# Performance work log

Hardware: AMD Instinct MI355X
Metric: run time of the kernel (lower is better)

The kernel has to match this reference:

```python
import jax, jax.numpy as jnp
import numpy as np

DIM_IN, DIM_OUT, DIM_HID = 1024, 1024, 1024
BATCH = 16384


def setup_inputs() -> dict:
    key = jax.random.key(0)
    k1, k2, k3, k4 = jax.random.split(key, 4)
    x = jax.random.normal(k1, (BATCH, DIM_IN), dtype=jnp.float32)
    # W_slow: Linear(dim_in -> dim_out + 2*dim_hidden + 1)
    W_slow_w = jax.random.normal(k2, (DIM_OUT + 2 * DIM_HID + 1, DIM_IN), dtype=jnp.float32) * (1.0 / np.sqrt(DIM_IN))
    W_slow_b = jax.random.normal(k3, (DIM_OUT + 2 * DIM_HID + 1,), dtype=jnp.float32) * 0.01
    # W_fast: Linear(dim_hidden -> dim_out), weight initialized to zero per module
    W_fast_w = jnp.zeros((DIM_OUT, DIM_HID), dtype=jnp.float32)
    W_fast_b = jax.random.normal(k4, (DIM_OUT,), dtype=jnp.float32) * 0.01
    return {"x": x, "W_slow_w": W_slow_w, "W_slow_b": W_slow_b,
            "W_fast_w": W_fast_w, "W_fast_b": W_fast_b}


def reference(x, W_slow_w, W_slow_b, W_fast_w, W_fast_b):
    B = x.shape[0]
    s = x @ W_slow_w.T + W_slow_b                      # [B, O + 2H + 1]
    k = s[:, :DIM_HID]                                 # [B, H]
    v = s[:, DIM_HID:DIM_HID + DIM_OUT]                # [B, O]
    q = s[:, DIM_HID + DIM_OUT:DIM_HID + DIM_OUT + DIM_HID]  # [B, H]
    lr = jax.nn.sigmoid(s[:, -1:])                     # [B, 1]
    # fast-weight read with softmax key
    v_bar = jax.nn.softmax(k, axis=1) @ W_fast_w.T + W_fast_b  # [B, O]
    # delta-rule outer-product update (batched, normalized by B)
    delta = jnp.einsum('bo,bh->oh', lr * (v - v_bar), jax.nn.sigmoid(k)) / B  # [O, H]
    W_new = W_fast_w + delta
    # read with updated fast weights
    return jax.nn.softmax(q, axis=1) @ W_new.T + W_fast_b  # [B, O]
```

## Files before the change

kernel.cpp:

```cpp
#include <hip/hip_runtime.h>
#include <math.h>

static constexpr int BATCH = 16384;

typedef __attribute__((ext_vector_type(8))) __bf16 bf16x8;
typedef __attribute__((ext_vector_type(4))) float f32x4;

__device__ __forceinline__ float sigm(float x) { return 1.0f / (1.0f + expf(-x)); }

__device__ __forceinline__ unsigned short f2bf(float f) {
  unsigned u = __float_as_uint(f);
  return (unsigned short)((u + 0x7fffu + ((u >> 16) & 1u)) >> 16);
}
__device__ __forceinline__ float bf2f(unsigned short u) {
  return __uint_as_float((unsigned)u << 16);
}

template <int EPI>
__global__ __launch_bounds__(512, 2) void mgemm8(
    const unsigned short* __restrict__ Ag, const unsigned short* __restrict__ Bg,
    int lda, int ldb, const float* __restrict__ bias,
    unsigned short* __restrict__ t0, unsigned short* __restrict__ t1,
    unsigned short* __restrict__ t2, float* __restrict__ Cf,
    const unsigned short* __restrict__ vTin, const float* __restrict__ lrp,
    unsigned short* __restrict__ outT, int ldT) {
  constexpr int NT = 32;
  __shared__ unsigned short As[4 * 8192];
  __shared__ unsigned short Bs[4 * 8192];
  const int tid = threadIdx.x, lane = tid & 63, w = tid >> 6;
  const int lm = lane & 15, kg = lane >> 4;
  const int wm = w >> 2, wn = w & 3;
  const int bm = blockIdx.y * 256, bn = blockIdx.x * 256;
  const int kz = (EPI == 3) ? (blockIdx.z << 10) : 0;
  f32x4 acc[8][4] = {};

  int offA[8], offB[4];
#pragma unroll
  for (int i = 0; i < 8; i++) {
    int r = wm * 128 + i * 16 + lm;
    offA[i] = r * 32 + (((kg + r + (r >> 2)) & 3) << 3);
  }
#pragma unroll
  for (int j = 0; j < 4; j++) {
    int r = wn * 64 + j * 16 + lm;
    offB[j] = r * 32 + (((kg + r + (r >> 2)) & 3) << 3);
  }
  const unsigned short* gA[2];
  const unsigned short* gB[2];
  int ldsoff[2];
#pragma unroll
  for (int i = 0; i < 2; i++) {
    int r = i * 128 + w * 16 + (lane >> 2);
    int q = ((lane & 3) - r - (r >> 2)) & 3;
    gA[i] = Ag + (size_t)(bm + r) * lda + kz + q * 8;
    gB[i] = Bg + (size_t)(bn + r) * ldb + kz + q * 8;
    ldsoff[i] = i * 4096 + w * 512;
  }
  auto stageA = [&](int tt, int buf) {
#pragma unroll
    for (int i = 0; i < 2; i++)
      __builtin_amdgcn_global_load_lds(
          (__attribute__((address_space(1))) void*)(unsigned short*)(gA[i] + tt * 32),
          (__attribute__((address_space(3))) void*)(As + buf * 8192 + ldsoff[i]),
          16, 0, 0);
  };
  auto stageB = [&](int tt, int buf) {
#pragma unroll
    for (int i = 0; i < 2; i++)
      __builtin_amdgcn_global_load_lds(
          (__attribute__((address_space(1))) void*)(unsigned short*)(gB[i] + tt * 32),
          (__attribute__((address_space(3))) void*)(Bs + buf * 8192 + ldsoff[i]),
          16, 0, 0);
  };

  stageA(0, 0); stageB(0, 0);
  stageA(1, 1); stageB(1, 1);
  asm volatile("s_waitcnt vmcnt(4)" ::: "memory");
  __builtin_amdgcn_s_barrier();
  __builtin_amdgcn_sched_barrier(0);

  for (int t = 0; t < NT; ++t) {
    const unsigned short* Ab = As + (t & 3) * 8192;
    const unsigned short* Bb = Bs + (t & 3) * 8192;
    bf16x8 aF[4], bF[4];
#pragma unroll
    for (int i = 0; i < 4; i++) aF[i] = *(const bf16x8*)(Ab + offA[i]);
#pragma unroll
    for (int j = 0; j < 4; j++) bF[j] = *(const bf16x8*)(Bb + offB[j]);
    if (t + 2 < NT) stageA(t + 2, (t + 2) & 3);
    __builtin_amdgcn_s_barrier();
    asm volatile("s_waitcnt lgkmcnt(0)" ::: "memory");
    __builtin_amdgcn_sched_barrier(0);
    __builtin_amdgcn_s_setprio(1);
#pragma unroll
    for (int i = 0; i < 4; i++)
#pragma unroll
      for (int j = 0; j < 4; j++)
        acc[i][j] = __builtin_amdgcn_mfma_f32_16x16x32_bf16(aF[i], bF[j], acc[i][j], 0, 0, 0);
    __builtin_amdgcn_s_setprio(0);
    __builtin_amdgcn_sched_barrier(0);
    __builtin_amdgcn_s_barrier();
    bf16x8 aG[4];
#pragma unroll
    for (int i = 0; i < 4; i++) aG[i] = *(const bf16x8*)(Ab + offA[4 + i]);
    if (t + 2 < NT) stageB(t + 2, (t + 2) & 3);
    __builtin_amdgcn_s_barrier();
    asm volatile("s_waitcnt lgkmcnt(0)" ::: "memory");
    __builtin_amdgcn_sched_barrier(0);
    __builtin_amdgcn_s_setprio(1);
#pragma unroll
    for (int i = 0; i < 4; i++)
#pragma unroll
      for (int j = 0; j < 4; j++)
        acc[4 + i][j] = __builtin_amdgcn_mfma_f32_16x16x32_bf16(aG[i], bF[j], acc[4 + i][j], 0, 0, 0);
    __builtin_amdgcn_s_setprio(0);
    __builtin_amdgcn_sched_barrier(0);
    if (t < NT - 2) { asm volatile("s_waitcnt vmcnt(4)" ::: "memory"); }
    else            { asm volatile("s_waitcnt vmcnt(0)" ::: "memory"); }
    __builtin_amdgcn_s_barrier();
    __builtin_amdgcn_sched_barrier(0);
  }

#pragma unroll
  for (int i = 0; i < 8; i++) {
#pragma unroll
    for (int j = 0; j < 4; j++) {
      const int gcol = bn + wn * 64 + j * 16 + lm;
      const int grow0 = bm + wm * 128 + i * 16 + kg * 4;
      if (EPI == 0) {
        const int which = gcol >> 10;
        unsigned short* dst = which == 0 ? t0 : (which == 1 ? t1 : t2);
        const float bv = bias[gcol];
        ushort4 pk;
        pk.x = f2bf(acc[i][j][0] + bv);
        pk.y = f2bf(acc[i][j][1] + bv);
        pk.z = f2bf(acc[i][j][2] + bv);
        pk.w = f2bf(acc[i][j][3] + bv);
        *(ushort4*)(dst + (size_t)(gcol & 1023) * ldT + grow0) = pk;
      } else if (EPI == 1) {
        const float bv = bias[gcol];
        const float4 l4 = *(const float4*)(lrp + grow0);
        const ushort4 v4 = *(const ushort4*)(vTin + (size_t)gcol * ldT + grow0);
        ushort4 o;
        o.x = f2bf(l4.x * (bf2f(v4.x) - (acc[i][j][0] + bv)));
        o.y = f2bf(l4.y * (bf2f(v4.y) - (acc[i][j][1] + bv)));
        o.z = f2bf(l4.z * (bf2f(v4.z) - (acc[i][j][2] + bv)));
        o.w = f2bf(l4.w * (bf2f(v4.w) - (acc[i][j][3] + bv)));
        *(ushort4*)(outT + (size_t)gcol * ldT + grow0) = o;
      } else if (EPI == 2) {
        const float bv = bias[gcol];
#pragma unroll
        for (int r = 0; r < 4; r++)
          Cf[(size_t)(grow0 + r) * 1024 + gcol] = acc[i][j][r] + bv;
      } else {
        float* dst = Cf + (size_t)blockIdx.z * (1024ull * 1024ull);
#pragma unroll
        for (int r = 0; r < 4; r++)
          dst[(size_t)(grow0 + r) * 1024 + gcol] = acc[i][j][r];
      }
    }
  }
}

template <int EPI>
__global__ __launch_bounds__(256) void mgemm(
    const unsigned short* __restrict__ Ag, const unsigned short* __restrict__ Bg,
    int lda, int ldb, int ksl, const float* __restrict__ bias,
    unsigned short* __restrict__ t0, unsigned short* __restrict__ t1,
    unsigned short* __restrict__ t2, float* __restrict__ Cf,
    const unsigned short* __restrict__ vTin, const float* __restrict__ lrp,
    unsigned short* __restrict__ outT, int ldT) {
  __shared__ unsigned short As[128 * 32];
  __shared__ unsigned short Bs[128 * 32];
  const int tid = threadIdx.x, lane = tid & 63, w = tid >> 6;
  const int lm = lane & 15, kg = lane >> 4;
  const int mh = (w >> 1) * 64, nh = (w & 1) * 64;
  const int bm = blockIdx.y * 128, bn = blockIdx.x * 128;
  const int kstart = blockIdx.z * ksl, kend = kstart + ksl;
  f32x4 acc[4][4] = {};

  int offA[4], offB[4];
#pragma unroll
  for (int i = 0; i < 4; i++) {
    int rA = mh + i * 16 + lm;
    offA[i] = rA * 32 + (((kg + rA + (rA >> 2)) & 3) << 3);
    int rB = nh + i * 16 + lm;
    offB[i] = rB * 32 + (((kg + rB + (rB >> 2)) & 3) << 3);
  }
  int rowS[2], kcS[2];
#pragma unroll
  for (int t = 0; t < 2; t++) {
    int c = (w * 2 + t) * 64 + lane;
    rowS[t] = c >> 2;
    kcS[t] = ((((c & 3) - rowS[t] - (rowS[t] >> 2)) & 3) << 3);
  }

  for (int k0 = kstart; k0 < kend; k0 += 32) {
#pragma unroll
    for (int t = 0; t < 2; t++) {
      __builtin_amdgcn_global_load_lds(
          (__attribute__((address_space(1))) void*)(unsigned short*)(
              Ag + (size_t)(bm + rowS[t]) * lda + k0 + kcS[t]),
          (__attribute__((address_space(3))) void*)(As + (w * 2 + t) * 512), 16, 0, 0);
      __builtin_amdgcn_global_load_lds(
          (__attribute__((address_space(1))) void*)(unsigned short*)(
              Bg + (size_t)(bn + rowS[t]) * ldb + k0 + kcS[t]),
          (__attribute__((address_space(3))) void*)(Bs + (w * 2 + t) * 512), 16, 0, 0);
    }
    __syncthreads();
    bf16x8 aF[4], bF[4];
#pragma unroll
    for (int i = 0; i < 4; i++) {
      aF[i] = *(const bf16x8*)(As + offA[i]);
      bF[i] = *(const bf16x8*)(Bs + offB[i]);
    }
#pragma unroll
    for (int i = 0; i < 4; i++)
#pragma unroll
      for (int j = 0; j < 4; j++)
        acc[i][j] = __builtin_amdgcn_mfma_f32_16x16x32_bf16(aF[i], bF[j], acc[i][j], 0, 0, 0);
    __syncthreads();
  }

#pragma unroll
  for (int i = 0; i < 4; i++) {
#pragma unroll
    for (int j = 0; j < 4; j++) {
      const int gcol = bn + nh + j * 16 + lm;
      const int grow0 = bm + mh + i * 16 + kg * 4;
      if (EPI == 3) {
        float* dst = Cf + (size_t)blockIdx.z * (1024ull * 1024ull);
#pragma unroll
        for (int r = 0; r < 4; r++)
          dst[(size_t)(grow0 + r) * 1024 + gcol] = acc[i][j][r];
      }
    }
  }
}

template <bool DOSIG>
__global__ __launch_bounds__(256) void tsoftmax(
    const unsigned short* __restrict__ in, int ldin,
    unsigned short* __restrict__ rowout,
    unsigned short* __restrict__ sigT, int ldT) {
  __shared__ unsigned short tile[1024 * 16];
  __shared__ float red[16 * 17];
  const int t = threadIdx.x, bl = t & 15, fg = t >> 4;
  const int B0 = blockIdx.x * 16;
  const int f0 = fg * 64;
  float ls = 0.f;
  for (int f = f0; f < f0 + 64; f++) {
    unsigned short u = in[(size_t)f * ldin + B0 + bl];
    tile[f * 16 + bl] = u;
    ls += expf(bf2f(u));
  }
  red[bl * 17 + fg] = ls;
  __syncthreads();
  float tot = 0.f;
#pragma unroll
  for (int g = 0; g < 16; g++) tot += red[bl * 17 + g];
  const float inv = 1.0f / tot;
  for (int fb = f0; fb < f0 + 64; fb += 4) {
    float v[4];
#pragma unroll
    for (int e = 0; e < 4; e++) v[e] = bf2f(tile[(fb + e) * 16 + bl]);
    ushort4 o;
    o.x = f2bf(expf(v[0]) * inv);
    o.y = f2bf(expf(v[1]) * inv);
    o.z = f2bf(expf(v[2]) * inv);
    o.w = f2bf(expf(v[3]) * inv);
    *(ushort4*)(rowout + (size_t)(B0 + bl) * 1024 + fb) = o;
    if (DOSIG) {
#pragma unroll
      for (int e = 0; e < 4; e++)
        sigT[(size_t)(fb + e) * ldT + B0 + bl] = f2bf(sigm(v[e]));
    }
  }
}

__global__ __launch_bounds__(256) void lrx(const float* __restrict__ x,
                                           const float* __restrict__ Wsw,
                                           const float* __restrict__ Wsb,
                                           float* __restrict__ lrOut,
                                           unsigned short* __restrict__ xbf) {
  const int lane = threadIdx.x & 63, w = threadIdx.x >> 6;
  const int b = blockIdx.x * 4 + w;
  const float* xr = x + (size_t)b * 1024;
  const float* wr = Wsw + 3072ull * 1024ull;
  float sum = 0.f;
#pragma unroll
  for (int j = 0; j < 4; j++) {
    int f = lane + 64 * j;
    float4 xv = ((const float4*)xr)[f];
    float4 wv = ((const float4*)wr)[f];
    sum += xv.x * wv.x + xv.y * wv.y + xv.z * wv.z + xv.w * wv.w;
    ushort4 o = {f2bf(xv.x), f2bf(xv.y), f2bf(xv.z), f2bf(xv.w)};
    ((ushort4*)(xbf + (size_t)b * 1024))[f] = o;
  }
#pragma unroll
  for (int o = 32; o; o >>= 1) sum += __shfl_down(sum, o, 64);
  if (lane == 0) lrOut[b] = sigm(sum + Wsb[3072]);
}

__global__ __launch_bounds__(256) void cvt_bf(const float* __restrict__ in,
                                              unsigned short* __restrict__ outp) {
  size_t i = (size_t)blockIdx.x * 256 + threadIdx.x;
  float4 v = ((const float4*)in)[i];
  ushort4 o = {f2bf(v.x), f2bf(v.y), f2bf(v.z), f2bf(v.w)};
  ((ushort4*)outp)[i] = o;
}

template <int NZ>
__global__ __launch_bounds__(256) void wnewk(const float* __restrict__ P,
                                             const float* __restrict__ Wfw,
                                             unsigned short* __restrict__ wnbf) {
  const size_t i = (size_t)blockIdx.x * 256 + threadIdx.x;
  float s = 0.f;
#pragma unroll
  for (int z = 0; z < NZ; z++) s += P[(size_t)z * (1024ull * 1024ull) + i];
  wnbf[i] = f2bf(Wfw[i] + s * (1.0f / 16384.0f));
}

extern "C" void kernel_launch(void* const* d_in, const int* in_sizes, int n_in,
                              void* d_out, int out_size, void* d_ws, size_t ws_size,
                              hipStream_t stream) {
  (void)in_sizes; (void)n_in; (void)out_size;
  const float* x   = (const float*)d_in[0];
  const float* Wsw = (const float*)d_in[1];
  const float* Wsb = (const float*)d_in[2];
  const float* Wfw = (const float*)d_in[3];
  const float* Wfb = (const float*)d_in[4];
  float* out = (float*)d_out;

  const size_t MB = 1ull << 20;
  int nc;
  if      (ws_size >= 216 * MB) nc = 1;
  else if (ws_size >= 164 * MB) nc = 2;
  else if (ws_size >= 122 * MB) nc = 4;
  else                          nc = 8;
  const size_t Bc = BATCH / nc;
  const int BcI = (int)Bc;
  const int zc = 8 / nc;
  const size_t CB = Bc * 1024 * 2;

  char* p = (char*)d_ws;
  size_t off = 0;
  auto alloc = [&](size_t bytes) {
    char* cur = p + off;
    off = (off + bytes + 255) & ~(size_t)255;
    return cur;
  };
  unsigned short* wbf  = (unsigned short*)alloc(3072ull * 1024 * 2);
  unsigned short* wfbf = (unsigned short*)alloc(1024ull * 1024 * 2);
  unsigned short* wnbf = (unsigned short*)alloc(1024ull * 1024 * 2);
  float*          lr   = (float*)alloc(BATCH * 4);
  unsigned short* qsm  = (unsigned short*)alloc((size_t)BATCH * 1024 * 2);

  unsigned short *xbf, *ksm, *kt, *Ut, *vT, *qt, *SKt;
  float* P;
  if (nc == 1) {
    char* rA = alloc(CB);
    char* rB = alloc(CB);
    char* rC = alloc(CB);
    char* rD = alloc(CB);
    char* rE = alloc(CB);
    xbf = (unsigned short*)rA; ksm = (unsigned short*)rA;
    kt  = (unsigned short*)rB; Ut  = (unsigned short*)rB;
    vT  = (unsigned short*)rC;
    qt  = (unsigned short*)rD;
    P   = (float*)rC;
    SKt = (unsigned short*)rE;
  } else {
    P   = (float*)alloc(32 * MB);
    char* rA = alloc(CB);
    char* rB = alloc(CB);
    xbf = (unsigned short*)rA; ksm = (unsigned short*)rA;
    kt  = (unsigned short*)rB; Ut  = (unsigned short*)rB;
    vT  = (unsigned short*)alloc(CB);
    qt  = (unsigned short*)alloc(CB);
    SKt = (unsigned short*)alloc(CB);
  }

  cvt_bf<<<dim3(3072), 256, 0, stream>>>(Wsw, wbf);
  cvt_bf<<<dim3(1024), 256, 0, stream>>>(Wfw, wfbf);

  for (int c = 0; c < nc; c++) {
    const float* xc = x + (size_t)c * Bc * 1024;
    float* lrc = lr + (size_t)c * Bc;
    lrx<<<dim3((unsigned)(Bc / 4)), 256, 0, stream>>>(xc, Wsw, Wsb, lrc, xbf);
    mgemm8<0><<<dim3(12, (unsigned)(Bc / 256)), 512, 0, stream>>>(
        xbf, wbf, 1024, 1024, Wsb, kt, vT, qt, nullptr, nullptr, nullptr,
        nullptr, BcI);
    tsoftmax<true><<<dim3((unsigned)(Bc / 16)), 256, 0, stream>>>(
        kt, BcI, ksm, SKt, BcI);
    tsoftmax<false><<<dim3((unsigned)(Bc / 16)), 256, 0, stream>>>(
        qt, BcI, qsm + (size_t)c * Bc * 1024, nullptr, BcI);
    mgemm8<1><<<dim3(4, (unsigned)(Bc / 256)), 512, 0, stream>>>(
        ksm, wfbf, 1024, 1024, Wfb, nullptr, nullptr, nullptr, nullptr,
        vT, lrc, Ut, BcI);
    if (nc == 1) {
      mgemm8<3><<<dim3(4, 4, 16), 512, 0, stream>>>(
          Ut, SKt, BcI, BcI, nullptr, nullptr, nullptr, nullptr,
          P, nullptr, nullptr, nullptr, BcI);
    } else {
      mgemm<3><<<dim3(8, 8, zc), 256, 0, stream>>>(
          Ut, SKt, BcI, BcI, 2048, nullptr, nullptr, nullptr, nullptr,
          P + (size_t)c * zc * 1024 * 1024, nullptr, nullptr, nullptr, BcI);
    }
  }

  if (nc == 1)
    wnewk<16><<<dim3(1024 * 1024 / 256), 256, 0, stream>>>(P, Wfw, wnbf);
  else
    wnewk<8><<<dim3(1024 * 1024 / 256), 256, 0, stream>>>(P, Wfw, wnbf);

  mgemm8<2><<<dim3(4, BATCH / 256), 512, 0, stream>>>(
      qsm, wnbf, 1024, 1024, Wfb, nullptr, nullptr, nullptr, out,
      nullptr, nullptr, nullptr, 0);
}
```

Measured before the change: 504.4 us.

## Prefetch second A fragment early, merge softmax and convert launches, vectorize wnew

In the main GEMM loop, the second half of the A fragments is now read from LDS together with the first half. The wait uses lgkmcnt(4) so the first MFMA batch can start while those reads are still in flight, and one barrier is dropped. The two softmax launches become one kernel with a 2D grid, the two bf16 conversion launches become one, and the weight-update kernel now processes float4 vectors with a quarter of the blocks. This cuts launch overhead and LDS latency stalls, at the cost of more registers held live and one fewer synchronization point.

Measured after the change: 533.2 us. +5.7%, slower.

```diff
diff --git a/kernel.cpp b/kernel.cpp
--- a/kernel.cpp
+++ b/kernel.cpp
@@ -82,14 +82,16 @@
   for (int t = 0; t < NT; ++t) {
     const unsigned short* Ab = As + (t & 3) * 8192;
     const unsigned short* Bb = Bs + (t & 3) * 8192;
-    bf16x8 aF[4], bF[4];
+    bf16x8 aF[4], bF[4], aG[4];
 #pragma unroll
     for (int i = 0; i < 4; i++) aF[i] = *(const bf16x8*)(Ab + offA[i]);
 #pragma unroll
     for (int j = 0; j < 4; j++) bF[j] = *(const bf16x8*)(Bb + offB[j]);
+#pragma unroll
+    for (int i = 0; i < 4; i++) aG[i] = *(const bf16x8*)(Ab + offA[4 + i]);
     if (t + 2 < NT) stageA(t + 2, (t + 2) & 3);
     __builtin_amdgcn_s_barrier();
-    asm volatile("s_waitcnt lgkmcnt(0)" ::: "memory");
+    asm volatile("s_waitcnt lgkmcnt(4)" ::: "memory");
     __builtin_amdgcn_sched_barrier(0);
     __builtin_amdgcn_s_setprio(1);
 #pragma unroll
@@ -100,11 +102,7 @@
     __builtin_amdgcn_s_setprio(0);
     __builtin_amdgcn_sched_barrier(0);
     __builtin_amdgcn_s_barrier();
-    bf16x8 aG[4];
-#pragma unroll
-    for (int i = 0; i < 4; i++) aG[i] = *(const bf16x8*)(Ab + offA[4 + i]);
     if (t + 2 < NT) stageB(t + 2, (t + 2) & 3);
-    __builtin_amdgcn_s_barrier();
     asm volatile("s_waitcnt lgkmcnt(0)" ::: "memory");
     __builtin_amdgcn_sched_barrier(0);
     __builtin_amdgcn_s_setprio(1);
@@ -238,13 +236,15 @@
   }
 }
 
-template <bool DOSIG>
-__global__ __launch_bounds__(256) void tsoftmax(
-    const unsigned short* __restrict__ in, int ldin,
-    unsigned short* __restrict__ rowout,
+__global__ __launch_bounds__(256) void tsoftmax2(
+    const unsigned short* __restrict__ inK, const unsigned short* __restrict__ inQ,
+    int ldin, unsigned short* __restrict__ outK, unsigned short* __restrict__ outQ,
     unsigned short* __restrict__ sigT, int ldT) {
   __shared__ unsigned short tile[1024 * 16];
   __shared__ float red[16 * 17];
+  const bool isK = blockIdx.y == 0;
+  const unsigned short* in = isK ? inK : inQ;
+  unsigned short* rowout = isK ? outK : outQ;
   const int t = threadIdx.x, bl = t & 15, fg = t >> 4;
   const int B0 = blockIdx.x * 16;
   const int f0 = fg * 64;
@@ -270,7 +270,7 @@
     o.z = f2bf(expf(v[2]) * inv);
     o.w = f2bf(expf(v[3]) * inv);
     *(ushort4*)(rowout + (size_t)(B0 + bl) * 1024 + fb) = o;
-    if (DOSIG) {
+    if (isK) {
 #pragma unroll
       for (int e = 0; e < 4; e++)
         sigT[(size_t)(fb + e) * ldT + B0 + bl] = f2bf(sigm(v[e]));
@@ -302,12 +302,17 @@
   if (lane == 0) lrOut[b] = sigm(sum + Wsb[3072]);
 }
 
-__global__ __launch_bounds__(256) void cvt_bf(const float* __restrict__ in,
-                                              unsigned short* __restrict__ outp) {
-  size_t i = (size_t)blockIdx.x * 256 + threadIdx.x;
-  float4 v = ((const float4*)in)[i];
+__global__ __launch_bounds__(256) void cvt2(const float* __restrict__ a,
+                                            const float* __restrict__ b,
+                                            unsigned short* __restrict__ oa,
+                                            unsigned short* __restrict__ ob) {
+  const bool first = blockIdx.x < 3072;
+  const float* src = first ? a : b;
+  unsigned short* dst = first ? oa : ob;
+  size_t i = (size_t)(first ? blockIdx.x : blockIdx.x - 3072) * 256 + threadIdx.x;
+  float4 v = ((const float4*)src)[i];
   ushort4 o = {f2bf(v.x), f2bf(v.y), f2bf(v.z), f2bf(v.w)};
-  ((ushort4*)outp)[i] = o;
+  ((ushort4*)dst)[i] = o;
 }
 
 template <int NZ>
@@ -315,10 +320,17 @@
                                              const float* __restrict__ Wfw,
                                              unsigned short* __restrict__ wnbf) {
   const size_t i = (size_t)blockIdx.x * 256 + threadIdx.x;
-  float s = 0.f;
-#pragma unroll
-  for (int z = 0; z < NZ; z++) s += P[(size_t)z * (1024ull * 1024ull) + i];
-  wnbf[i] = f2bf(Wfw[i] + s * (1.0f / 16384.0f));
+  float4 s = {0.f, 0.f, 0.f, 0.f};
+#pragma unroll
+  for (int z = 0; z < NZ; z++) {
+    float4 v = ((const float4*)(P + (size_t)z * (1024ull * 1024ull)))[i];
+    s.x += v.x; s.y += v.y; s.z += v.z; s.w += v.w;
+  }
+  float4 wv = ((const float4*)Wfw)[i];
+  const float r = 1.0f / 16384.0f;
+  ushort4 o = {f2bf(wv.x + s.x * r), f2bf(wv.y + s.y * r),
+               f2bf(wv.z + s.z * r), f2bf(wv.w + s.w * r)};
+  ((ushort4*)wnbf)[i] = o;
 }
 
 extern "C" void kernel_launch(void* const* d_in, const int* in_sizes, int n_in,
@@ -381,8 +393,7 @@
     SKt = (unsigned short*)alloc(CB);
   }
 
-  cvt_bf<<<dim3(3072), 256, 0, stream>>>(Wsw, wbf);
-  cvt_bf<<<dim3(1024), 256, 0, stream>>>(Wfw, wfbf);
+  cvt2<<<dim3(4096), 256, 0, stream>>>(Wsw, Wfw, wbf, wfbf);
 
   for (int c = 0; c < nc; c++) {
     const float* xc = x + (size_t)c * Bc * 1024;
@@ -391,10 +402,8 @@
     mgemm8<0><<<dim3(12, (unsigned)(Bc / 256)), 512, 0, stream>>>(
         xbf, wbf, 1024, 1024, Wsb, kt, vT, qt, nullptr, nullptr, nullptr,
         nullptr, BcI);
-    tsoftmax<true><<<dim3((unsigned)(Bc / 16)), 256, 0, stream>>>(
-        kt, BcI, ksm, SKt, BcI);
-    tsoftmax<false><<<dim3((unsigned)(Bc / 16)), 256, 0, stream>>>(
-        qt, BcI, qsm + (size_t)c * Bc * 1024, nullptr, BcI);
+    tsoftmax2<<<dim3((unsigned)(Bc / 16), 2), 256, 0, stream>>>(
+        kt, qt, BcI, ksm, qsm + (size_t)c * Bc * 1024, SKt, BcI);
     mgemm8<1><<<dim3(4, (unsigned)(Bc / 256)), 512, 0, stream>>>(
         ksm, wfbf, 1024, 1024, Wfb, nullptr, nullptr, nullptr, nullptr,
         vT, lrc, Ut, BcI);
@@ -410,9 +419,9 @@
   }
 
   if (nc == 1)
-    wnewk<16><<<dim3(1024 * 1024 / 256), 256, 0, stream>>>(P, Wfw, wnbf);
+    wnewk<16><<<dim3(1024), 256, 0, stream>>>(P, Wfw, wnbf);
   else
-    wnewk<8><<<dim3(1024 * 1024 / 256), 256, 0, stream>>>(P, Wfw, wnbf);
+    wnewk<8><<<dim3(1024), 256, 0, stream>>>(P, Wfw, wnbf);
 
   mgemm8<2><<<dim3(4, BATCH / 256), 512, 0, stream>>>(
       qsm, wnbf, 1024, 1024, Wfb, nullptr, nullptr, nullptr, out,
```
